# Kernel tuning notes

Hardware: AMD Instinct MI355X
Metric: run time of the kernel (lower is better)

Reference implementation:

```python
import jax, jax.numpy as jnp
import numpy as np

B, S, D, H = 16, 577, 1280, 16
HD = D // H  # 80
HALF = HD // 2  # 40


def setup_inputs() -> dict:
    key = jax.random.key(0)
    ks = jax.random.split(key, 8)
    hidden_states = jax.random.normal(ks[0], (B, S, D), dtype=jnp.float32)
    # 2D rotary frequencies: random angles -> unit-magnitude complex rotations
    angles = jax.random.uniform(ks[1], (S, HALF), dtype=jnp.float32) * (2.0 * np.pi)
    freqs_cos = jnp.cos(angles)
    freqs_sin = jnp.sin(angles)
    scale = 1.0 / np.sqrt(D)
    Wq = jax.random.normal(ks[2], (D, D), dtype=jnp.float32) * scale
    Wk = jax.random.normal(ks[3], (D, D), dtype=jnp.float32) * scale
    Wv = jax.random.normal(ks[4], (D, D), dtype=jnp.float32) * scale
    Wo = jax.random.normal(ks[5], (D, D), dtype=jnp.float32) * scale
    z = jnp.zeros((D,), dtype=jnp.float32)
    return {
        "hidden_states": hidden_states,
        "freqs_cos": freqs_cos,
        "freqs_sin": freqs_sin,
        "Wq": Wq, "bq": z, "Wk": Wk, "bk": z,
        "Wv": Wv, "bv": z, "Wo": Wo, "bo": z,
    }


def _apply_rotary(x, cos, sin):
    # x: [B,S,H,HD]; cos/sin: [S, HD/2]; interleaved complex pairs (even=real, odd=imag)
    xr = x[..., 0::2]
    xi = x[..., 1::2]
    c = cos[None, :, None, :]
    s = sin[None, :, None, :]
    out_r = xr * c - xi * s
    out_i = xr * s + xi * c
    # re-interleave pairs back to [..., HD]
    return jnp.stack([out_r, out_i], axis=-1).reshape(x.shape)


def reference(hidden_states, freqs_cos, freqs_sin, Wq, bq, Wk, bk, Wv, bv, Wo, bo):
    q = (hidden_states @ Wq.T + bq).reshape(B, S, H, HD)
    k = (hidden_states @ Wk.T + bk).reshape(B, S, H, HD)
    v = (hidden_states @ Wv.T + bv).reshape(B, S, H, HD)
    q = _apply_rotary(q, freqs_cos, freqs_sin)
    k = _apply_rotary(k, freqs_cos, freqs_sin)
    # [B,H,S,HD]
    q = q.transpose(0, 2, 1, 3)
    k = k.transpose(0, 2, 1, 3)
    v = v.transpose(0, 2, 1, 3)
    scale = 1.0 / np.sqrt(HD).astype(np.float32)
    scores = jnp.einsum("bhsd,bhtd->bhst", q, k) * scale
    probs = jax.nn.softmax(scores, axis=-1)
    attn = jnp.einsum("bhst,bhtd->bhsd", probs, v)
    attn = attn.transpose(0, 2, 1, 3).reshape(B, S, D)
    return attn @ Wo.T + bo
```

## Files before the change

### kernel.cpp

```cpp
#include <hip/hip_runtime.h>

#define B_N 16
#define S_N 577
#define D_N 1280
#define H_N 16
#define HD_N 80
#define HALF_N 40
#define M_N 9232
#define M_PAD 9344
#define K_N 1280
#define VT_S 608
#define QSCALE 0.11180339887498949f

typedef __bf16 bf16_t;
typedef bf16_t bf16x8 __attribute__((ext_vector_type(8)));
typedef float f32x4 __attribute__((ext_vector_type(4)));

__device__ __forceinline__ float bf2f(unsigned short u) {
    union { unsigned int i; float f; } x; x.i = ((unsigned int)u) << 16; return x.f;
}
__device__ __forceinline__ unsigned short f2bf(float f) {
    union { unsigned int i; float f; } x; x.f = f;
    unsigned int r = x.i + 0x7FFFu + ((x.i >> 16) & 1u);
    return (unsigned short)(r >> 16);
}

__device__ __forceinline__ void gld_lds16(const unsigned short* g, unsigned short* l) {
    __builtin_amdgcn_global_load_lds(
        (const __attribute__((address_space(1))) unsigned int*)g,
        (__attribute__((address_space(3))) unsigned int*)l,
        16, 0, 0);
}

__global__ __launch_bounds__(256) void cvt_kernel(const float* __restrict__ in,
                                                  unsigned short* __restrict__ out, int n4) {
    int i = blockIdx.x * 256 + threadIdx.x;
    if (i < n4) {
        float4 v = ((const float4*)in)[i];
        ushort4 o;
        o.x = f2bf(v.x); o.y = f2bf(v.y); o.z = f2bf(v.z); o.w = f2bf(v.w);
        ((ushort4*)out)[i] = o;
    }
}

#define W4_N (D_N * K_N / 4)
__global__ __launch_bounds__(256) void cvt4_kernel(
    const float* __restrict__ w0, const float* __restrict__ w1,
    const float* __restrict__ w2, const float* __restrict__ w3,
    unsigned short* __restrict__ out) {
    int i = blockIdx.x * 256 + threadIdx.x;
    if (i >= 4 * W4_N) return;
    int r = i / W4_N, j = i - r * W4_N;
    const float* src = (r == 0) ? w0 : (r == 1) ? w1 : (r == 2) ? w2 : w3;
    float4 v = ((const float4*)src)[j];
    ushort4 o;
    o.x = f2bf(v.x); o.y = f2bf(v.y); o.z = f2bf(v.z); o.w = f2bf(v.w);
    ((ushort4*)out)[i] = o;
}

template <int MODE>
__global__ __launch_bounds__(256) void mgemm64_kernel(
    const unsigned short* __restrict__ A,
    const unsigned short* __restrict__ Wb,
    const float* __restrict__ b0, const float* __restrict__ b1,
    const float* __restrict__ b2,
    const float* __restrict__ cosb, const float* __restrict__ sinb,
    void* __restrict__ o0, void* __restrict__ o1, void* __restrict__ o2)
{
    __shared__ __align__(16) unsigned short As[128 * 64];
    __shared__ __align__(16) unsigned short Bs[128 * 64];

    const int tid = threadIdx.x;
    const int wave = tid >> 6, lane = tid & 63;
    const int quad = lane >> 4, n = lane & 15;
    const int wm = wave >> 1, wn = wave & 1;
    const int m0 = blockIdx.y * 128, n0g = blockIdx.x * 128;

    const int srow = lane >> 3;
    const int scol = (((lane & 7) ^ srow) * 8);

    const unsigned short* gA = A + (size_t)(m0 + wave * 32 + srow) * K_N + scol;
    const unsigned short* gB = Wb + (size_t)(n0g + wave * 32 + srow) * K_N + scol;
    unsigned short* lA = As + wave * 32 * 64;
    unsigned short* lB = Bs + wave * 32 * 64;

    f32x4 acc[4][4] = {};

    for (int k0 = 0; k0 < K_N; k0 += 64) {
        #pragma unroll
        for (int i = 0; i < 4; ++i) {
            gld_lds16(gA + k0 + i * 8 * K_N, lA + i * 512);
            gld_lds16(gB + k0 + i * 8 * K_N, lB + i * 512);
        }
        __syncthreads();

        #pragma unroll
        for (int kk = 0; kk < 2; ++kk) {
            const int sa = ((((kk << 2) | quad) ^ (n & 7)) * 8);
            bf16x8 af[4], bfr[4];
            #pragma unroll
            for (int mt = 0; mt < 4; ++mt)
                af[mt] = *(const bf16x8*)&As[(wm * 64 + mt * 16 + n) * 64 + sa];
            #pragma unroll
            for (int nt = 0; nt < 4; ++nt)
                bfr[nt] = *(const bf16x8*)&Bs[(wn * 64 + nt * 16 + n) * 64 + sa];
            #pragma unroll
            for (int mt = 0; mt < 4; ++mt)
                #pragma unroll
                for (int nt = 0; nt < 4; ++nt)
                    acc[mt][nt] = __builtin_amdgcn_mfma_f32_16x16x32_bf16(
                        af[mt], bfr[nt], acc[mt][nt], 0, 0, 0);
        }
        __syncthreads();
    }

    const int mbase = m0 + wm * 64;

    if (MODE == 3) {
        const int nbase = n0g + wn * 64;
        float* out = (float*)o0;
        #pragma unroll
        for (int mt = 0; mt < 4; ++mt)
            #pragma unroll
            for (int nt = 0; nt < 4; ++nt) {
                const int ncol = nbase + nt * 16 + n;
                const float bv = b0[ncol];
                #pragma unroll
                for (int r = 0; r < 4; ++r) {
                    int mrow = mbase + mt * 16 + quad * 4 + r;
                    if (mrow < M_N)
                        out[(size_t)mrow * D_N + ncol] = acc[mt][nt][r] + bv;
                }
            }
    } else {
        const int wsel = blockIdx.x / 10;
        const float* bias = (wsel == 0) ? b0 : (wsel == 1) ? b1 : b2;
        unsigned short* out =
            (unsigned short*)((wsel == 0) ? o0 : (wsel == 1) ? o1 : o2);
        const int nloc = n0g - wsel * 1280 + wn * 64;
        const bool evn = (n & 1) == 0;
        #pragma unroll
        for (int nt = 0; nt < 4; ++nt) {
            const int ncol = nloc + nt * 16 + n;
            const int h = ncol / HD_N, hd = ncol - h * HD_N;
            const float bv = bias[ncol];
            #pragma unroll
            for (int mt = 0; mt < 4; ++mt)
                #pragma unroll
                for (int r = 0; r < 4; ++r) {
                    int mrow = mbase + mt * 16 + quad * 4 + r;
                    int b = mrow / S_N, s = mrow - b * S_N;
                    float v = acc[mt][nt][r] + bv;
                    if (wsel == 2) {
                        if (mrow < M_N)
                            out[((size_t)(b * H_N + h) * HD_N + hd) * VT_S + s] =
                                f2bf(v);
                    } else {
                        float pv = __shfl_xor(v, 1);
                        float c  = cosb[s * HALF_N + (hd >> 1)];
                        float sn = sinb[s * HALF_N + (hd >> 1)];
                        float res = evn ? (v * c - pv * sn) : (pv * sn + v * c);
                        if (wsel == 0) res *= QSCALE;
                        if (mrow < M_N)
                            out[((size_t)(b * H_N + h) * S_N + s) * HD_N + hd] =
                                f2bf(res);
                    }
                }
        }
    }
}

__global__ __launch_bounds__(256) void fattn_kernel(
    const unsigned short* __restrict__ qb,
    const unsigned short* __restrict__ kb,
    const unsigned short* __restrict__ vt,
    unsigned short* __restrict__ attn)
{
    __shared__ __align__(16) unsigned short Plds[4][2][2][16 * 32];

    const int tid = threadIdx.x;
    const int wave = tid >> 6, lane = tid & 63;
    const int quad = lane >> 4, n = lane & 15;

    const int bid = blockIdx.x;
    const int xcd = bid & 7, t = bid >> 3;
    const int qt = t % 5, hl = t / 5;
    const int bh = hl * 8 + xcd;
    const int q0 = qt * 128 + wave * 32;

    const bf16x8 zf{};
    const unsigned short* qrow0 = qb + ((size_t)bh * S_N + q0 + n) * HD_N;
    const unsigned short* qrow1 = qrow0 + 16 * HD_N;
    bf16x8 aq00 = *(const bf16x8*)(qrow0 + quad * 8);
    bf16x8 aq01 = *(const bf16x8*)(qrow0 + 32 + quad * 8);
    bf16x8 aq02 = (quad < 2) ? *(const bf16x8*)(qrow0 + 64 + quad * 8) : zf;
    bf16x8 aq10 = *(const bf16x8*)(qrow1 + quad * 8);
    bf16x8 aq11 = *(const bf16x8*)(qrow1 + 32 + quad * 8);
    bf16x8 aq12 = (quad < 2) ? *(const bf16x8*)(qrow1 + 64 + quad * 8) : zf;

    const bf16_t one = (bf16_t)1.0f;
    const bf16x8 vones_all = {one, one, one, one, one, one, one, one};
    const bf16x8 vones = (n == 0) ? vones_all : zf;

    f32x4 o0[6] = {};
    f32x4 o1[6] = {};

    const unsigned short* kbase = kb + (size_t)bh * S_N * HD_N;
    const unsigned short* vbase = vt + (size_t)bh * HD_N * VT_S;

    #pragma unroll 2
    for (int t0 = 0; t0 < 608; t0 += 32) {
        const int pp = (t0 >> 5) & 1;
        unsigned short* pl0 = &Plds[wave][pp][0][0];
        unsigned short* pl1 = &Plds[wave][pp][1][0];

        const unsigned short* krA = kbase + (size_t)(t0 + n) * HD_N;
        const unsigned short* krB = krA + 16 * HD_N;
        bf16x8 bA0 = *(const bf16x8*)(krA + quad * 8);
        bf16x8 bA1 = *(const bf16x8*)(krA + 32 + quad * 8);
        bf16x8 bA2 = (quad < 2) ? *(const bf16x8*)(krA + 64 + quad * 8) : zf;
        bf16x8 bB0 = *(const bf16x8*)(krB + quad * 8);
        bf16x8 bB1 = *(const bf16x8*)(krB + 32 + quad * 8);
        bf16x8 bB2 = (quad < 2) ? *(const bf16x8*)(krB + 64 + quad * 8) : zf;

        f32x4 c00{}, c01{}, c10{}, c11{};
        c00 = __builtin_amdgcn_mfma_f32_16x16x32_bf16(aq00, bA0, c00, 0, 0, 0);
        c00 = __builtin_amdgcn_mfma_f32_16x16x32_bf16(aq01, bA1, c00, 0, 0, 0);
        c00 = __builtin_amdgcn_mfma_f32_16x16x32_bf16(aq02, bA2, c00, 0, 0, 0);
        c01 = __builtin_amdgcn_mfma_f32_16x16x32_bf16(aq00, bB0, c01, 0, 0, 0);
        c01 = __builtin_amdgcn_mfma_f32_16x16x32_bf16(aq01, bB1, c01, 0, 0, 0);
        c01 = __builtin_amdgcn_mfma_f32_16x16x32_bf16(aq02, bB2, c01, 0, 0, 0);
        c10 = __builtin_amdgcn_mfma_f32_16x16x32_bf16(aq10, bA0, c10, 0, 0, 0);
        c10 = __builtin_amdgcn_mfma_f32_16x16x32_bf16(aq11, bA1, c10, 0, 0, 0);
        c10 = __builtin_amdgcn_mfma_f32_16x16x32_bf16(aq12, bA2, c10, 0, 0, 0);
        c11 = __builtin_amdgcn_mfma_f32_16x16x32_bf16(aq10, bB0, c11, 0, 0, 0);
        c11 = __builtin_amdgcn_mfma_f32_16x16x32_bf16(aq11, bB1, c11, 0, 0, 0);
        c11 = __builtin_amdgcn_mfma_f32_16x16x32_bf16(aq12, bB2, c11, 0, 0, 0);

        const bool mA = (t0 + n) >= S_N;
        const bool mB = (t0 + 16 + n) >= S_N;

        #pragma unroll
        for (int r = 0; r < 4; ++r) {
            float p00 = mA ? 0.0f : __expf(c00[r]);
            float p01 = mB ? 0.0f : __expf(c01[r]);
            float p10 = mA ? 0.0f : __expf(c10[r]);
            float p11 = mB ? 0.0f : __expf(c11[r]);
            pl0[(quad * 4 + r) * 32 + n]      = f2bf(p00);
            pl0[(quad * 4 + r) * 32 + 16 + n] = f2bf(p01);
            pl1[(quad * 4 + r) * 32 + n]      = f2bf(p10);
            pl1[(quad * 4 + r) * 32 + 16 + n] = f2bf(p11);
        }

        bf16x8 ap0 = *(const bf16x8*)(pl0 + n * 32 + quad * 8);
        bf16x8 ap1 = *(const bf16x8*)(pl1 + n * 32 + quad * 8);

        #pragma unroll
        for (int nt = 0; nt < 5; ++nt) {
            const unsigned short* vr = vbase + (size_t)(nt * 16 + n) * VT_S + t0 + quad * 8;
            bf16x8 bv = *(const bf16x8*)vr;
            o0[nt] = __builtin_amdgcn_mfma_f32_16x16x32_bf16(ap0, bv, o0[nt], 0, 0, 0);
            o1[nt] = __builtin_amdgcn_mfma_f32_16x16x32_bf16(ap1, bv, o1[nt], 0, 0, 0);
        }
        o0[5] = __builtin_amdgcn_mfma_f32_16x16x32_bf16(ap0, vones, o0[5], 0, 0, 0);
        o1[5] = __builtin_amdgcn_mfma_f32_16x16x32_bf16(ap1, vones, o1[5], 0, 0, 0);
    }

    const int b = bh >> 4, h = bh & 15;
    #pragma unroll
    for (int r = 0; r < 4; ++r) {
        float l0 = __shfl(o0[5][r], lane & 48);
        float l1 = __shfl(o1[5][r], lane & 48);
        float linv0 = 1.0f / l0, linv1 = 1.0f / l1;
        int s0 = q0 + quad * 4 + r;
        int s1 = s0 + 16;
        #pragma unroll
        for (int nt = 0; nt < 5; ++nt) {
            if (s0 < S_N)
                attn[((size_t)b * S_N + s0) * D_N + h * HD_N + nt * 16 + n] =
                    f2bf(o0[nt][r] * linv0);
            if (s1 < S_N)
                attn[((size_t)b * S_N + s1) * D_N + h * HD_N + nt * 16 + n] =
                    f2bf(o1[nt][r] * linv1);
        }
    }
}

extern "C" void kernel_launch(void* const* d_in, const int* in_sizes, int n_in,
                              void* d_out, int out_size, void* d_ws, size_t ws_size,
                              hipStream_t stream) {
    const float* hs = (const float*)d_in[0];
    const float* fc = (const float*)d_in[1];
    const float* fs = (const float*)d_in[2];
    const float* Wq = (const float*)d_in[3];
    const float* bq = (const float*)d_in[4];
    const float* Wk = (const float*)d_in[5];
    const float* bk = (const float*)d_in[6];
    const float* Wv = (const float*)d_in[7];
    const float* bv = (const float*)d_in[8];
    const float* Wo = (const float*)d_in[9];
    const float* bo = (const float*)d_in[10];
    float* out = (float*)d_out;

    char* ws = (char*)d_ws;
    size_t off = 0;
    auto alloc = [&](size_t bytes) {
        char* p = ws + off; off += (bytes + 255) & ~(size_t)255; return p;
    };
    unsigned short* hsb  = (unsigned short*)alloc((size_t)M_PAD * K_N * 2);
    unsigned short* qb   = (unsigned short*)alloc((size_t)M_N * K_N * 2 + 32768);
    unsigned short* kb   = (unsigned short*)alloc((size_t)M_N * K_N * 2 + 32768);
    unsigned short* vt   = (unsigned short*)alloc((size_t)B_N * H_N * HD_N * VT_S * 2);
    unsigned short* Wall = (unsigned short*)alloc((size_t)4 * D_N * K_N * 2);

    const int HS4 = M_N * K_N / 4;
    dim3 blk(256);

    cvt_kernel<<<(HS4 + 255) / 256, blk, 0, stream>>>(hs, hsb, HS4);
    cvt4_kernel<<<(4 * W4_N + 255) / 256, blk, 0, stream>>>(Wq, Wk, Wv, Wo, Wall);

    mgemm64_kernel<4><<<dim3(30, 73), blk, 0, stream>>>(
        hsb, Wall, bq, bk, bv, fc, fs, qb, kb, vt);

    fattn_kernel<<<dim3(1280), blk, 0, stream>>>(qb, kb, vt, hsb );

    mgemm64_kernel<3><<<dim3(10, 73), blk, 0, stream>>>(
        hsb, Wall + 3 * (size_t)D_N * K_N, bo, bo, bo, fc, fs, out, out, out);
}
```

Before: 458.3 us.

## Double-buffer LDS tiles in the bf16 GEMM to overlap loads with MFMA

Splits the shared-memory A/B tiles into two ping-pong buffers. The global-to-LDS load of the next K slice is issued before the MFMA work on the current slice, with one wait and barrier per iteration instead of two. The goal is to hide global memory latency behind matrix-core compute. It doubles LDS use per block, which may lower occupancy, and the K loop is now fully unrolled.

After: 485.0 us. 1.06x slower.

```diff
diff --git a/kernel.cpp b/kernel.cpp
--- a/kernel.cpp
+++ b/kernel.cpp
@@ -67,8 +67,8 @@
     const float* __restrict__ cosb, const float* __restrict__ sinb,
     void* __restrict__ o0, void* __restrict__ o1, void* __restrict__ o2)
 {
-    __shared__ __align__(16) unsigned short As[128 * 64];
-    __shared__ __align__(16) unsigned short Bs[128 * 64];
+    __shared__ __align__(16) unsigned short As[2][128 * 64];
+    __shared__ __align__(16) unsigned short Bs[2][128 * 64];
 
     const int tid = threadIdx.x;
     const int wave = tid >> 6, lane = tid & 63;
@@ -81,29 +81,31 @@
 
     const unsigned short* gA = A + (size_t)(m0 + wave * 32 + srow) * K_N + scol;
     const unsigned short* gB = Wb + (size_t)(n0g + wave * 32 + srow) * K_N + scol;
-    unsigned short* lA = As + wave * 32 * 64;
-    unsigned short* lB = Bs + wave * 32 * 64;
+    const int lofs = wave * 32 * 64;
 
     f32x4 acc[4][4] = {};
 
-    for (int k0 = 0; k0 < K_N; k0 += 64) {
+    auto stage = [&](int pp, int k0) {
+        unsigned short* lA = &As[pp][lofs];
+        unsigned short* lB = &Bs[pp][lofs];
         #pragma unroll
         for (int i = 0; i < 4; ++i) {
             gld_lds16(gA + k0 + i * 8 * K_N, lA + i * 512);
             gld_lds16(gB + k0 + i * 8 * K_N, lB + i * 512);
         }
-        __syncthreads();
-
+    };
+
+    auto compute = [&](int pp) {
         #pragma unroll
         for (int kk = 0; kk < 2; ++kk) {
             const int sa = ((((kk << 2) | quad) ^ (n & 7)) * 8);
             bf16x8 af[4], bfr[4];
             #pragma unroll
             for (int mt = 0; mt < 4; ++mt)
-                af[mt] = *(const bf16x8*)&As[(wm * 64 + mt * 16 + n) * 64 + sa];
+                af[mt] = *(const bf16x8*)&As[pp][(wm * 64 + mt * 16 + n) * 64 + sa];
             #pragma unroll
             for (int nt = 0; nt < 4; ++nt)
-                bfr[nt] = *(const bf16x8*)&Bs[(wn * 64 + nt * 16 + n) * 64 + sa];
+                bfr[nt] = *(const bf16x8*)&Bs[pp][(wn * 64 + nt * 16 + n) * 64 + sa];
             #pragma unroll
             for (int mt = 0; mt < 4; ++mt)
                 #pragma unroll
@@ -111,8 +113,21 @@
                     acc[mt][nt] = __builtin_amdgcn_mfma_f32_16x16x32_bf16(
                         af[mt], bfr[nt], acc[mt][nt], 0, 0, 0);
         }
-        __syncthreads();
-    }
+    };
+
+    stage(0, 0);
+    asm volatile("s_waitcnt vmcnt(0)" ::: "memory");
+    __builtin_amdgcn_s_barrier();
+
+    #pragma unroll
+    for (int t = 0; t < 19; ++t) {
+        const int pp = t & 1;
+        stage(pp ^ 1, (t + 1) * 64);
+        compute(pp);
+        asm volatile("s_waitcnt vmcnt(0)" ::: "memory");
+        __builtin_amdgcn_s_barrier();
+    }
+    compute(1);
 
     const int mbase = m0 + wm * 64;
 
```
